# Kernel tuning notes

Measured on AMD Instinct MI355X. Metric: run time of the kernel, lower is better.

The kernel has to match this reference:

```python
import jax, jax.numpy as jnp
import numpy as np

DIM = 768
HEADS = 12
HEAD_DIM = DIM // HEADS
SCALE = HEAD_DIM ** -0.5


def setup_inputs() -> dict:
    key = jax.random.key(0)
    ks = jax.random.split(key, 5)
    x = jax.random.normal(ks[0], (2, 4096, DIM), dtype=jnp.float32)
    # torch nn.Linear params: weight [out, in], bias [out]
    qkv_w = jax.random.normal(ks[1], (3 * DIM, DIM), dtype=jnp.float32) * (DIM ** -0.5)
    qkv_b = jax.random.normal(ks[2], (3 * DIM,), dtype=jnp.float32) * 0.02
    proj_w = jax.random.normal(ks[3], (DIM, DIM), dtype=jnp.float32) * (DIM ** -0.5)
    proj_b = jax.random.normal(ks[4], (DIM,), dtype=jnp.float32) * 0.02
    return {"x": x, "qkv_w": qkv_w, "qkv_b": qkv_b, "proj_w": proj_w, "proj_b": proj_b}


def reference(x, qkv_w, qkv_b, proj_w, proj_b):
    b, n, c = x.shape
    qkv = x @ qkv_w.T + qkv_b                      # [b, n, 3c]
    qkv = qkv.reshape(b, n, 3, HEADS, HEAD_DIM)
    qkv = jnp.transpose(qkv, (2, 0, 3, 1, 4))      # [3, b, h, n, d]
    q, k, v = qkv[0], qkv[1], qkv[2]
    attn = jax.nn.softmax(jnp.einsum('bhqd,bhkd->bhqk', q, k) * SCALE, axis=-1)
    out = jnp.einsum('bhqk,bhkd->bhqd', attn, v)   # [b, h, n, d]
    out = jnp.transpose(out, (0, 2, 1, 3)).reshape(b, n, c)
    return out @ proj_w.T + proj_b
```

## Files before the change

### kernel.cpp

```cpp
#include <hip/hip_runtime.h>
#include <stdint.h>

#define SEQ   4096
#define NDIM  768
#define HD    64
#define NH    12
#define NBH   24
#define MTOT  8192

#define LSTR 40
#define PSTR 72

typedef short s8v __attribute__((ext_vector_type(8)));
typedef float f4v __attribute__((ext_vector_type(4)));
typedef float f16x __attribute__((ext_vector_type(16)));
typedef unsigned short u16;
typedef u16 u16x4 __attribute__((ext_vector_type(4)));
typedef uint32_t u32x4v __attribute__((ext_vector_type(4)));
typedef int i32x2 __attribute__((ext_vector_type(2)));

#define C1 0.18033688011112042f

__device__ __forceinline__ u16 f2bf(float f) {
  union { float f; uint32_t u; } cv; cv.f = f;
  const uint32_t u = cv.u;
  return (u16)((u + 0x7fffu + ((u >> 16) & 1u)) >> 16);
}
__device__ __forceinline__ float ex2(float x) { return __builtin_amdgcn_exp2f(x); }

__device__ __forceinline__ uint32_t cvtpk_bf16(float lo, float hi) {
  uint32_t r;
  asm("v_cvt_pk_bf16_f32 %0, %1, %2" : "=v"(r) : "v"(lo), "v"(hi));
  return r;
}
__device__ __forceinline__ void pl32swap(uint32_t& a, uint32_t& b) {
  i32x2 r = __builtin_amdgcn_permlane32_swap((int)a, (int)b, false, false);
  a = (uint32_t)r.x; b = (uint32_t)r.y;
}

__global__ __launch_bounds__(256) void cvt3_kernel(
    const float* __restrict__ a, u16* __restrict__ da, int na4,
    const float* __restrict__ b, u16* __restrict__ db, int nb4,
    const float* __restrict__ c, u16* __restrict__ dc, int nc4) {
  int i = blockIdx.x * 256 + threadIdx.x;
  const float* s; u16* d;
  if (i < na4)             { s = a; d = da; }
  else if (i < na4 + nb4)  { s = b; d = db; i -= na4; }
  else if (i < na4 + nb4 + nc4) { s = c; d = dc; i -= na4 + nb4; }
  else return;
  const float4 f = ((const float4*)s)[i];
  u16x4 r;
  r[0] = f2bf(f.x); r[1] = f2bf(f.y); r[2] = f2bf(f.z); r[3] = f2bf(f.w);
  ((u16x4*)d)[i] = r;
}

__global__ __launch_bounds__(256) void gemm_qkv(const u16* __restrict__ A,
    const u16* __restrict__ B, const float* __restrict__ bias,
    u16* __restrict__ qg, u16* __restrict__ kg, u16* __restrict__ vtg) {
  __shared__ __align__(16) u16 at[128 * LSTR];
  __shared__ __align__(16) u16 bt[128 * LSTR];
  const int tid  = threadIdx.x;
  const int lane = tid & 63;
  const int w    = tid >> 6;
  const int quad = lane >> 4;
  const int col  = lane & 15;
  const int m0 = blockIdx.y * 128;
  const int n0 = blockIdx.x * 128;
  const int srow = tid >> 2;
  const int sch  = (tid & 3) * 8;
  const int wm = (w >> 1) * 64;
  const int wn = (w & 1) * 64;

  const f4v fz = {0.f, 0.f, 0.f, 0.f};
  f4v acc[4][4];
#pragma unroll
  for (int i = 0; i < 4; i++)
#pragma unroll
    for (int j = 0; j < 4; j++) acc[i][j] = fz;

  const u16* ap0 = A + (size_t)(m0 + srow) * NDIM + sch;
  const u16* ap1 = A + (size_t)(m0 + 64 + srow) * NDIM + sch;
  const u16* bp0 = B + (size_t)(n0 + srow) * NDIM + sch;
  const u16* bp1 = B + (size_t)(n0 + 64 + srow) * NDIM + sch;

  for (int k0 = 0; k0 < NDIM; k0 += 32) {
    const s8v va0 = *(const s8v*)(ap0 + k0);
    const s8v va1 = *(const s8v*)(ap1 + k0);
    const s8v vb0 = *(const s8v*)(bp0 + k0);
    const s8v vb1 = *(const s8v*)(bp1 + k0);
    __syncthreads();
    *(s8v*)(at + srow * LSTR + sch) = va0;
    *(s8v*)(at + (64 + srow) * LSTR + sch) = va1;
    *(s8v*)(bt + srow * LSTR + sch) = vb0;
    *(s8v*)(bt + (64 + srow) * LSTR + sch) = vb1;
    __syncthreads();
    s8v af[4], bf[4];
#pragma unroll
    for (int i = 0; i < 4; i++)
      af[i] = *(const s8v*)(at + (wm + i * 16 + col) * LSTR + quad * 8);
#pragma unroll
    for (int j = 0; j < 4; j++)
      bf[j] = *(const s8v*)(bt + (wn + j * 16 + col) * LSTR + quad * 8);
#pragma unroll
    for (int i = 0; i < 4; i++)
#pragma unroll
      for (int j = 0; j < 4; j++)
        acc[i][j] = __builtin_amdgcn_mfma_f32_16x16x32_bf16(af[i], bf[j], acc[i][j], 0, 0, 0);
  }

  const int wmg = m0 + wm;
  const int wng = n0 + wn;
  const int s = n0 / NDIM;
#pragma unroll
  for (int j = 0; j < 4; j++) {
    const int c = wng + j * 16 + col;
    const float bv = bias[c];
    const int r = c - s * NDIM;
    const int h = r >> 6;
    const int d = r & 63;
#pragma unroll
    for (int i = 0; i < 4; i++) {
      const int mb = wmg + i * 16 + quad * 4;
      const int bb = mb >> 12;
      const int n  = mb & 4095;
      const size_t hb = (size_t)(bb * NH + h);
      const f4v v = acc[i][j];
      if (s == 2) {
        u16x4 pk;
#pragma unroll
        for (int rg = 0; rg < 4; rg++) pk[rg] = f2bf(v[rg] + bv);
        *(u16x4*)(vtg + (hb * HD + d) * SEQ + n) = pk;
      } else if (s == 0) {
#pragma unroll
        for (int rg = 0; rg < 4; rg++)
          qg[(hb * SEQ + (size_t)(n + rg)) * HD + d] = f2bf((v[rg] + bv) * C1);
      } else {
#pragma unroll
        for (int rg = 0; rg < 4; rg++)
          kg[(hb * SEQ + (size_t)(n + rg)) * HD + d] = f2bf(v[rg] + bv);
      }
    }
  }
}

__global__ __launch_bounds__(256, 3) void attn_kernel(const u16* __restrict__ qg,
    const u16* __restrict__ kg, const u16* __restrict__ vtg, u16* __restrict__ og) {
  __shared__ __align__(16) u16 kls[2][64 * PSTR];
  __shared__ __align__(16) u16 vls[2][64 * PSTR];
  __shared__ float lws[4][32];

  const int tid  = threadIdx.x;
  const int lane = tid & 63;
  const int w    = tid >> 6;
  const int hi   = lane >> 5;
  const int c    = lane & 31;
  const int blk = blockIdx.x;
  const int bh  = blk % NBH;
  const int q0  = (blk / NBH) * 128;
  const size_t gbase = (size_t)bh * (SEQ * HD);
  const int wq = w * 32;

  s8v qf[4];
#pragma unroll
  for (int s = 0; s < 4; s++)
    qf[s] = *(const s8v*)(qg + gbase + (size_t)(q0 + wq + c) * HD + s * 16 + hi * 8);

  f16x o0, o1;
#pragma unroll
  for (int e = 0; e < 16; e++) { o0[e] = 0.f; o1[e] = 0.f; }
  float l0 = 0.f, l1 = 0.f, l2 = 0.f, l3 = 0.f;

  const int srow8 = tid >> 3;
  const int sch8  = (tid & 7) * 8;
  const u16* kp = kg  + gbase + (size_t)srow8 * HD  + sch8;
  const u16* vp = vtg + gbase + (size_t)srow8 * SEQ;

  s8v kr0 = *(const s8v*)(kp);
  s8v kr1 = *(const s8v*)(kp + (size_t)32 * HD);
  s8v vr0 = *(const s8v*)(vp + sch8);
  s8v vr1 = *(const s8v*)(vp + (size_t)32 * SEQ + sch8);
  *(s8v*)(kls[0] + srow8 * PSTR + sch8) = kr0;
  *(s8v*)(kls[0] + (32 + srow8) * PSTR + sch8) = kr1;
  *(s8v*)(vls[0] + srow8 * PSTR + sch8) = vr0;
  *(s8v*)(vls[0] + (32 + srow8) * PSTR + sch8) = vr1;

  for (int kb = 0; kb < SEQ; kb += 64) {
    const int cur = (kb >> 6) & 1;
    const u16* kt_ = kls[cur];
    const u16* vt_ = vls[cur];
    __syncthreads();

    if (kb + 64 < SEQ) {
      kr0 = *(const s8v*)(kp + (size_t)(kb + 64) * HD);
      kr1 = *(const s8v*)(kp + (size_t)(kb + 96) * HD);
      vr0 = *(const s8v*)(vp + kb + 64 + sch8);
      vr1 = *(const s8v*)(vp + (size_t)32 * SEQ + kb + 64 + sch8);
    }

    f16x st0, st1;
#pragma unroll
    for (int e = 0; e < 16; e++) { st0[e] = 0.f; st1[e] = 0.f; }
#pragma unroll
    for (int s = 0; s < 4; s++) {
      const s8v k0 = *(const s8v*)(kt_ + c * PSTR + s * 16 + hi * 8);
      const s8v k1 = *(const s8v*)(kt_ + (32 + c) * PSTR + s * 16 + hi * 8);
      st0 = __builtin_amdgcn_mfma_f32_32x32x16_bf16(k0, qf[s], st0, 0, 0, 0);
      st1 = __builtin_amdgcn_mfma_f32_32x32x16_bf16(k1, qf[s], st1, 0, 0, 0);
    }

    s8v pa0, pa1, pa2, pa3;
    {
      float p[16];
#pragma unroll
      for (int e = 0; e < 16; e++) p[e] = ex2(st0[e]);
      l0 += p[0] + p[4] + p[8]  + p[12];
      l1 += p[1] + p[5] + p[9]  + p[13];
      l2 += p[2] + p[6] + p[10] + p[14];
      l3 += p[3] + p[7] + p[11] + p[15];
      uint32_t k0 = cvtpk_bf16(p[0],  p[1]);
      uint32_t k1 = cvtpk_bf16(p[2],  p[3]);
      uint32_t k2 = cvtpk_bf16(p[4],  p[5]);
      uint32_t k3 = cvtpk_bf16(p[6],  p[7]);
      uint32_t k4 = cvtpk_bf16(p[8],  p[9]);
      uint32_t k5 = cvtpk_bf16(p[10], p[11]);
      uint32_t k6 = cvtpk_bf16(p[12], p[13]);
      uint32_t k7 = cvtpk_bf16(p[14], p[15]);
      pl32swap(k0, k2); pl32swap(k1, k3);
      pl32swap(k4, k6); pl32swap(k5, k7);
      u32x4v wA = {k0, k1, k2, k3};
      u32x4v wB = {k4, k5, k6, k7};
      pa0 = __builtin_bit_cast(s8v, wA);
      pa1 = __builtin_bit_cast(s8v, wB);
    }
    {
      float p[16];
#pragma unroll
      for (int e = 0; e < 16; e++) p[e] = ex2(st1[e]);
      l0 += p[0] + p[4] + p[8]  + p[12];
      l1 += p[1] + p[5] + p[9]  + p[13];
      l2 += p[2] + p[6] + p[10] + p[14];
      l3 += p[3] + p[7] + p[11] + p[15];
      uint32_t k0 = cvtpk_bf16(p[0],  p[1]);
      uint32_t k1 = cvtpk_bf16(p[2],  p[3]);
      uint32_t k2 = cvtpk_bf16(p[4],  p[5]);
      uint32_t k3 = cvtpk_bf16(p[6],  p[7]);
      uint32_t k4 = cvtpk_bf16(p[8],  p[9]);
      uint32_t k5 = cvtpk_bf16(p[10], p[11]);
      uint32_t k6 = cvtpk_bf16(p[12], p[13]);
      uint32_t k7 = cvtpk_bf16(p[14], p[15]);
      pl32swap(k0, k2); pl32swap(k1, k3);
      pl32swap(k4, k6); pl32swap(k5, k7);
      u32x4v wA = {k0, k1, k2, k3};
      u32x4v wB = {k4, k5, k6, k7};
      pa2 = __builtin_bit_cast(s8v, wA);
      pa3 = __builtin_bit_cast(s8v, wB);
    }

#pragma unroll
    for (int ks = 0; ks < 4; ks++) {
      const s8v pv = ks == 0 ? pa0 : ks == 1 ? pa1 : ks == 2 ? pa2 : pa3;
      const s8v v0 = *(const s8v*)(vt_ + c * PSTR + ks * 16 + hi * 8);
      const s8v v1 = *(const s8v*)(vt_ + (32 + c) * PSTR + ks * 16 + hi * 8);
      o0 = __builtin_amdgcn_mfma_f32_32x32x16_bf16(pv, v0, o0, 0, 0, 0);
      o1 = __builtin_amdgcn_mfma_f32_32x32x16_bf16(pv, v1, o1, 0, 0, 0);
    }

    if (kb + 64 < SEQ) {
      u16* kn = (u16*)kls[cur ^ 1];
      u16* vn = (u16*)vls[cur ^ 1];
      *(s8v*)(kn + srow8 * PSTR + sch8) = kr0;
      *(s8v*)(kn + (32 + srow8) * PSTR + sch8) = kr1;
      *(s8v*)(vn + srow8 * PSTR + sch8) = vr0;
      *(s8v*)(vn + (32 + srow8) * PSTR + sch8) = vr1;
    }
  }

  float lt = l0 + l1 + l2 + l3;
  lt += __shfl_xor(lt, 32);
  const float inv = 1.0f / lt;
  if (hi == 0) lws[w][c] = inv;

  const int b = bh / NH;
  const int h = bh % NH;
  u16* obase = og + (size_t)(b * SEQ + q0 + wq) * NDIM + h * HD + c;
#pragma unroll
  for (int r = 0; r < 16; r++) {
    const int row = (r & 3) + 8 * (r >> 2) + 4 * hi;
    const float invr = lws[w][row];
    u16* rp = obase + (size_t)row * NDIM;
    rp[0]  = f2bf(o0[r] * invr);
    rp[32] = f2bf(o1[r] * invr);
  }
}

__global__ __launch_bounds__(256) void gemm_proj(const u16* __restrict__ A,
    const u16* __restrict__ B, const float* __restrict__ bias, float* __restrict__ out) {
  __shared__ __align__(16) u16 at[128 * LSTR];
  __shared__ __align__(16) u16 bt[128 * LSTR];
  const int tid  = threadIdx.x;
  const int lane = tid & 63;
  const int w    = tid >> 6;
  const int quad = lane >> 4;
  const int col  = lane & 15;
  const int m0 = blockIdx.y * 128;
  const int n0 = blockIdx.x * 128;
  const int srow = tid >> 2;
  const int sch  = (tid & 3) * 8;
  const int wm = (w >> 1) * 64;
  const int wn = (w & 1) * 64;

  const f4v fz = {0.f, 0.f, 0.f, 0.f};
  f4v acc[4][4];
#pragma unroll
  for (int i = 0; i < 4; i++)
#pragma unroll
    for (int j = 0; j < 4; j++) acc[i][j] = fz;

  const u16* ap0 = A + (size_t)(m0 + srow) * NDIM + sch;
  const u16* ap1 = A + (size_t)(m0 + 64 + srow) * NDIM + sch;
  const u16* bp0 = B + (size_t)(n0 + srow) * NDIM + sch;
  const u16* bp1 = B + (size_t)(n0 + 64 + srow) * NDIM + sch;

  for (int k0 = 0; k0 < NDIM; k0 += 32) {
    const s8v va0 = *(const s8v*)(ap0 + k0);
    const s8v va1 = *(const s8v*)(ap1 + k0);
    const s8v vb0 = *(const s8v*)(bp0 + k0);
    const s8v vb1 = *(const s8v*)(bp1 + k0);
    __syncthreads();
    *(s8v*)(at + srow * LSTR + sch) = va0;
    *(s8v*)(at + (64 + srow) * LSTR + sch) = va1;
    *(s8v*)(bt + srow * LSTR + sch) = vb0;
    *(s8v*)(bt + (64 + srow) * LSTR + sch) = vb1;
    __syncthreads();
    s8v af[4], bf[4];
#pragma unroll
    for (int i = 0; i < 4; i++)
      af[i] = *(const s8v*)(at + (wm + i * 16 + col) * LSTR + quad * 8);
#pragma unroll
    for (int j = 0; j < 4; j++)
      bf[j] = *(const s8v*)(bt + (wn + j * 16 + col) * LSTR + quad * 8);
#pragma unroll
    for (int i = 0; i < 4; i++)
#pragma unroll
      for (int j = 0; j < 4; j++)
        acc[i][j] = __builtin_amdgcn_mfma_f32_16x16x32_bf16(af[i], bf[j], acc[i][j], 0, 0, 0);
  }

  const int wmg = m0 + wm;
  const int wng = n0 + wn;
#pragma unroll
  for (int j = 0; j < 4; j++) {
    const int c = wng + j * 16 + col;
    const float bv = bias[c];
#pragma unroll
    for (int i = 0; i < 4; i++) {
#pragma unroll
      for (int rg = 0; rg < 4; rg++)
        out[(size_t)(wmg + i * 16 + quad * 4 + rg) * NDIM + c] = acc[i][j][rg] + bv;
    }
  }
}

extern "C" void kernel_launch(void* const* d_in, const int* in_sizes, int n_in,
                              void* d_out, int out_size, void* d_ws, size_t ws_size,
                              hipStream_t stream) {
  const float* x      = (const float*)d_in[0];
  const float* qkv_w  = (const float*)d_in[1];
  const float* qkv_b  = (const float*)d_in[2];
  const float* proj_w = (const float*)d_in[3];
  const float* proj_b = (const float*)d_in[4];
  float* out = (float*)d_out;

  u16* ws   = (u16*)d_ws;
  u16* x_bf = ws;
  u16* wq   = x_bf + (size_t)MTOT * NDIM;
  u16* wp   = wq + (size_t)3 * NDIM * NDIM;
  u16* q_bf = wp + (size_t)NDIM * NDIM;
  u16* k_bf = q_bf + (size_t)NBH * SEQ * HD;
  u16* vt   = k_bf + (size_t)NBH * SEQ * HD;
  u16* a_bf = vt + (size_t)NBH * SEQ * HD;

  const int nx = MTOT * NDIM / 4, nw1 = 3 * NDIM * NDIM / 4, nw2 = NDIM * NDIM / 4;
  const int ntot = nx + nw1 + nw2;
  cvt3_kernel<<<(ntot + 255) / 256, 256, 0, stream>>>(x, x_bf, nx, qkv_w, wq, nw1,
                                                      proj_w, wp, nw2);

  gemm_qkv<<<dim3(18, 64), 256, 0, stream>>>(x_bf, wq, qkv_b, q_bf, k_bf, vt);
  attn_kernel<<<768, 256, 0, stream>>>(q_bf, k_bf, vt, a_bf);
  gemm_proj<<<dim3(6, 64), 256, 0, stream>>>(a_bf, wp, proj_b, out);
}
```

Measured before the change: 285.2 us.

## Load K fragments directly into registers and interleave softmax with PV MFMAs

K tiles are no longer staged through shared memory. Each lane loads its MFMA K fragments straight from global memory into registers, one tile ahead, which removes the K LDS stores and reads and halves shared-memory use. The PV matmul is split into two halves that are interleaved with the exp/convert work of each score block, and the MFMA sections are wrapped in s_setprio to favour matrix issue. The cost is more global-load traffic per wave, since lanes read overlapping K rows without reuse across waves, plus extra register pressure from the eight prefetched K fragments.

```diff
diff --git a/kernel.cpp b/kernel.cpp
--- a/kernel.cpp
+++ b/kernel.cpp
@@ -145,7 +145,6 @@
 
 __global__ __launch_bounds__(256, 3) void attn_kernel(const u16* __restrict__ qg,
     const u16* __restrict__ kg, const u16* __restrict__ vtg, u16* __restrict__ og) {
-  __shared__ __align__(16) u16 kls[2][64 * PSTR];
   __shared__ __align__(16) u16 vls[2][64 * PSTR];
   __shared__ float lws[4][32];
 
@@ -165,47 +164,58 @@
   for (int s = 0; s < 4; s++)
     qf[s] = *(const s8v*)(qg + gbase + (size_t)(q0 + wq + c) * HD + s * 16 + hi * 8);
 
-  f16x o0, o1;
-#pragma unroll
-  for (int e = 0; e < 16; e++) { o0[e] = 0.f; o1[e] = 0.f; }
+  const u16* kq0 = kg + gbase + (size_t)c * HD + hi * 8;
+  const u16* kq1 = kq0 + (size_t)32 * HD;
+  s8v kf0[4], kf1[4];
+#pragma unroll
+  for (int s = 0; s < 4; s++) {
+    kf0[s] = *(const s8v*)(kq0 + s * 16);
+    kf1[s] = *(const s8v*)(kq1 + s * 16);
+  }
+
+  f16x zacc;
+#pragma unroll
+  for (int e = 0; e < 16; e++) zacc[e] = 0.f;
+  f16x o0 = zacc, o1 = zacc;
   float l0 = 0.f, l1 = 0.f, l2 = 0.f, l3 = 0.f;
 
   const int srow8 = tid >> 3;
   const int sch8  = (tid & 7) * 8;
-  const u16* kp = kg  + gbase + (size_t)srow8 * HD  + sch8;
   const u16* vp = vtg + gbase + (size_t)srow8 * SEQ;
 
-  s8v kr0 = *(const s8v*)(kp);
-  s8v kr1 = *(const s8v*)(kp + (size_t)32 * HD);
   s8v vr0 = *(const s8v*)(vp + sch8);
   s8v vr1 = *(const s8v*)(vp + (size_t)32 * SEQ + sch8);
-  *(s8v*)(kls[0] + srow8 * PSTR + sch8) = kr0;
-  *(s8v*)(kls[0] + (32 + srow8) * PSTR + sch8) = kr1;
   *(s8v*)(vls[0] + srow8 * PSTR + sch8) = vr0;
   *(s8v*)(vls[0] + (32 + srow8) * PSTR + sch8) = vr1;
 
   for (int kb = 0; kb < SEQ; kb += 64) {
     const int cur = (kb >> 6) & 1;
-    const u16* kt_ = kls[cur];
     const u16* vt_ = vls[cur];
     __syncthreads();
 
     if (kb + 64 < SEQ) {
-      kr0 = *(const s8v*)(kp + (size_t)(kb + 64) * HD);
-      kr1 = *(const s8v*)(kp + (size_t)(kb + 96) * HD);
       vr0 = *(const s8v*)(vp + kb + 64 + sch8);
       vr1 = *(const s8v*)(vp + (size_t)32 * SEQ + kb + 64 + sch8);
     }
 
-    f16x st0, st1;
-#pragma unroll
-    for (int e = 0; e < 16; e++) { st0[e] = 0.f; st1[e] = 0.f; }
-#pragma unroll
-    for (int s = 0; s < 4; s++) {
-      const s8v k0 = *(const s8v*)(kt_ + c * PSTR + s * 16 + hi * 8);
-      const s8v k1 = *(const s8v*)(kt_ + (32 + c) * PSTR + s * 16 + hi * 8);
-      st0 = __builtin_amdgcn_mfma_f32_32x32x16_bf16(k0, qf[s], st0, 0, 0, 0);
-      st1 = __builtin_amdgcn_mfma_f32_32x32x16_bf16(k1, qf[s], st1, 0, 0, 0);
+    __builtin_amdgcn_s_setprio(1);
+    f16x st0 = __builtin_amdgcn_mfma_f32_32x32x16_bf16(kf0[0], qf[0], zacc, 0, 0, 0);
+    f16x st1 = __builtin_amdgcn_mfma_f32_32x32x16_bf16(kf1[0], qf[0], zacc, 0, 0, 0);
+#pragma unroll
+    for (int s = 1; s < 4; s++) {
+      st0 = __builtin_amdgcn_mfma_f32_32x32x16_bf16(kf0[s], qf[s], st0, 0, 0, 0);
+      st1 = __builtin_amdgcn_mfma_f32_32x32x16_bf16(kf1[s], qf[s], st1, 0, 0, 0);
+    }
+    __builtin_amdgcn_s_setprio(0);
+
+    if (kb + 64 < SEQ) {
+      const u16* nk0 = kq0 + (size_t)(kb + 64) * HD;
+      const u16* nk1 = kq1 + (size_t)(kb + 64) * HD;
+#pragma unroll
+      for (int s = 0; s < 4; s++) {
+        kf0[s] = *(const s8v*)(nk0 + s * 16);
+        kf1[s] = *(const s8v*)(nk1 + s * 16);
+      }
     }
 
     s8v pa0, pa1, pa2, pa3;
@@ -232,6 +242,20 @@
       pa0 = __builtin_bit_cast(s8v, wA);
       pa1 = __builtin_bit_cast(s8v, wB);
     }
+
+    __builtin_amdgcn_s_setprio(1);
+    {
+      const s8v v00 = *(const s8v*)(vt_ + c * PSTR + hi * 8);
+      const s8v v01 = *(const s8v*)(vt_ + (32 + c) * PSTR + hi * 8);
+      const s8v v10 = *(const s8v*)(vt_ + c * PSTR + 16 + hi * 8);
+      const s8v v11 = *(const s8v*)(vt_ + (32 + c) * PSTR + 16 + hi * 8);
+      o0 = __builtin_amdgcn_mfma_f32_32x32x16_bf16(pa0, v00, o0, 0, 0, 0);
+      o1 = __builtin_amdgcn_mfma_f32_32x32x16_bf16(pa0, v01, o1, 0, 0, 0);
+      o0 = __builtin_amdgcn_mfma_f32_32x32x16_bf16(pa1, v10, o0, 0, 0, 0);
+      o1 = __builtin_amdgcn_mfma_f32_32x32x16_bf16(pa1, v11, o1, 0, 0, 0);
+    }
+    __builtin_amdgcn_s_setprio(0);
+
     {
       float p[16];
 #pragma unroll
@@ -256,23 +280,24 @@
       pa3 = __builtin_bit_cast(s8v, wB);
     }
 
-#pragma unroll
-    for (int ks = 0; ks < 4; ks++) {
-      const s8v pv = ks == 0 ? pa0 : ks == 1 ? pa1 : ks == 2 ? pa2 : pa3;
-      const s8v v0 = *(const s8v*)(vt_ + c * PSTR + ks * 16 + hi * 8);
-      const s8v v1 = *(const s8v*)(vt_ + (32 + c) * PSTR + ks * 16 + hi * 8);
-      o0 = __builtin_amdgcn_mfma_f32_32x32x16_bf16(pv, v0, o0, 0, 0, 0);
-      o1 = __builtin_amdgcn_mfma_f32_32x32x16_bf16(pv, v1, o1, 0, 0, 0);
-    }
-
     if (kb + 64 < SEQ) {
-      u16* kn = (u16*)kls[cur ^ 1];
       u16* vn = (u16*)vls[cur ^ 1];
-      *(s8v*)(kn + srow8 * PSTR + sch8) = kr0;
-      *(s8v*)(kn + (32 + srow8) * PSTR + sch8) = kr1;
       *(s8v*)(vn + srow8 * PSTR + sch8) = vr0;
       *(s8v*)(vn + (32 + srow8) * PSTR + sch8) = vr1;
     }
+
+    __builtin_amdgcn_s_setprio(1);
+    {
+      const s8v v20 = *(const s8v*)(vt_ + c * PSTR + 32 + hi * 8);
+      const s8v v21 = *(const s8v*)(vt_ + (32 + c) * PSTR + 32 + hi * 8);
+      const s8v v30 = *(const s8v*)(vt_ + c * PSTR + 48 + hi * 8);
+      const s8v v31 = *(const s8v*)(vt_ + (32 + c) * PSTR + 48 + hi * 8);
+      o0 = __builtin_amdgcn_mfma_f32_32x32x16_bf16(pa2, v20, o0, 0, 0, 0);
+      o1 = __builtin_amdgcn_mfma_f32_32x32x16_bf16(pa2, v21, o1, 0, 0, 0);
+      o0 = __builtin_amdgcn_mfma_f32_32x32x16_bf16(pa3, v30, o0, 0, 0, 0);
+      o1 = __builtin_amdgcn_mfma_f32_32x32x16_bf16(pa3, v31, o1, 0, 0, 0);
+    }
+    __builtin_amdgcn_s_setprio(0);
   }
 
   float lt = l0 + l1 + l2 + l3;
```

Result: slower. 358.3 us (+25.6%).

## Use direct global-to-LDS loads with XOR swizzle in GEMMs and interleave PV MFMAs

Applied to the files above, without the earlier changes.

Both projection GEMMs now stage tiles with global_load_lds (16-byte direct-to-LDS loads), which bypasses VGPRs. The tiles use an unpadded XOR-swizzled layout to avoid bank conflicts. In the attention kernel, the P·V MFMAs are split into two halves interleaved with the second softmax exp block and the next-tile LDS stores, and the MFMA phases are wrapped in s_setprio. The goal is lower staging overhead and better overlap of MFMA with VALU work. The GEMM loop still waits synchronously on each load with no prefetch, and the direct LDS load relies on the swizzle mapping and per-wave base being right.

```diff
diff --git a/kernel.cpp b/kernel.cpp
--- a/kernel.cpp
+++ b/kernel.cpp
@@ -8,7 +8,6 @@
 #define NBH   24
 #define MTOT  8192
 
-#define LSTR 40
 #define PSTR 72
 
 typedef short s8v __attribute__((ext_vector_type(8)));
@@ -36,6 +35,11 @@
 __device__ __forceinline__ void pl32swap(uint32_t& a, uint32_t& b) {
   i32x2 r = __builtin_amdgcn_permlane32_swap((int)a, (int)b, false, false);
   a = (uint32_t)r.x; b = (uint32_t)r.y;
+}
+__device__ __forceinline__ void gload_lds16(const void* g, void* l) {
+  __builtin_amdgcn_global_load_lds(
+      (const __attribute__((address_space(1))) uint32_t*)g,
+      (__attribute__((address_space(3))) uint32_t*)l, 16, 0, 0);
 }
 
 __global__ __launch_bounds__(256) void cvt3_kernel(
@@ -57,8 +61,8 @@
 __global__ __launch_bounds__(256) void gemm_qkv(const u16* __restrict__ A,
     const u16* __restrict__ B, const float* __restrict__ bias,
     u16* __restrict__ qg, u16* __restrict__ kg, u16* __restrict__ vtg) {
-  __shared__ __align__(16) u16 at[128 * LSTR];
-  __shared__ __align__(16) u16 bt[128 * LSTR];
+  __shared__ __align__(16) u16 at[128 * 32];
+  __shared__ __align__(16) u16 bt[128 * 32];
   const int tid  = threadIdx.x;
   const int lane = tid & 63;
   const int w    = tid >> 6;
@@ -67,9 +71,10 @@
   const int m0 = blockIdx.y * 128;
   const int n0 = blockIdx.x * 128;
   const int srow = tid >> 2;
-  const int sch  = (tid & 3) * 8;
+  const int schk = ((tid & 3) ^ (srow & 3)) * 8;
   const int wm = (w >> 1) * 64;
   const int wn = (w & 1) * 64;
+  const int xq = (quad ^ (col & 3)) * 8;
 
   const f4v fz = {0.f, 0.f, 0.f, 0.f};
   f4v acc[4][4];
@@ -78,29 +83,27 @@
 #pragma unroll
     for (int j = 0; j < 4; j++) acc[i][j] = fz;
 
-  const u16* ap0 = A + (size_t)(m0 + srow) * NDIM + sch;
-  const u16* ap1 = A + (size_t)(m0 + 64 + srow) * NDIM + sch;
-  const u16* bp0 = B + (size_t)(n0 + srow) * NDIM + sch;
-  const u16* bp1 = B + (size_t)(n0 + 64 + srow) * NDIM + sch;
+  const u16* ga0 = A + (size_t)(m0 + srow) * NDIM + schk;
+  const u16* ga1 = A + (size_t)(m0 + 64 + srow) * NDIM + schk;
+  const u16* gb0 = B + (size_t)(n0 + srow) * NDIM + schk;
+  const u16* gb1 = B + (size_t)(n0 + 64 + srow) * NDIM + schk;
+  u16* const la = at + (size_t)w * 512;
+  u16* const lb = bt + (size_t)w * 512;
 
   for (int k0 = 0; k0 < NDIM; k0 += 32) {
-    const s8v va0 = *(const s8v*)(ap0 + k0);
-    const s8v va1 = *(const s8v*)(ap1 + k0);
-    const s8v vb0 = *(const s8v*)(bp0 + k0);
-    const s8v vb1 = *(const s8v*)(bp1 + k0);
     __syncthreads();
-    *(s8v*)(at + srow * LSTR + sch) = va0;
-    *(s8v*)(at + (64 + srow) * LSTR + sch) = va1;
-    *(s8v*)(bt + srow * LSTR + sch) = vb0;
-    *(s8v*)(bt + (64 + srow) * LSTR + sch) = vb1;
+    gload_lds16(ga0 + k0, la);
+    gload_lds16(ga1 + k0, la + 2048);
+    gload_lds16(gb0 + k0, lb);
+    gload_lds16(gb1 + k0, lb + 2048);
     __syncthreads();
     s8v af[4], bf[4];
 #pragma unroll
     for (int i = 0; i < 4; i++)
-      af[i] = *(const s8v*)(at + (wm + i * 16 + col) * LSTR + quad * 8);
+      af[i] = *(const s8v*)(at + (wm + i * 16 + col) * 32 + xq);
 #pragma unroll
     for (int j = 0; j < 4; j++)
-      bf[j] = *(const s8v*)(bt + (wn + j * 16 + col) * LSTR + quad * 8);
+      bf[j] = *(const s8v*)(bt + (wn + j * 16 + col) * 32 + xq);
 #pragma unroll
     for (int i = 0; i < 4; i++)
 #pragma unroll
@@ -200,6 +203,7 @@
     f16x st0, st1;
 #pragma unroll
     for (int e = 0; e < 16; e++) { st0[e] = 0.f; st1[e] = 0.f; }
+    __builtin_amdgcn_s_setprio(1);
 #pragma unroll
     for (int s = 0; s < 4; s++) {
       const s8v k0 = *(const s8v*)(kt_ + c * PSTR + s * 16 + hi * 8);
@@ -207,6 +211,7 @@
       st0 = __builtin_amdgcn_mfma_f32_32x32x16_bf16(k0, qf[s], st0, 0, 0, 0);
       st1 = __builtin_amdgcn_mfma_f32_32x32x16_bf16(k1, qf[s], st1, 0, 0, 0);
     }
+    __builtin_amdgcn_s_setprio(0);
 
     s8v pa0, pa1, pa2, pa3;
     {
@@ -232,6 +237,20 @@
       pa0 = __builtin_bit_cast(s8v, wA);
       pa1 = __builtin_bit_cast(s8v, wB);
     }
+
+    __builtin_amdgcn_s_setprio(1);
+    {
+      const s8v v00 = *(const s8v*)(vt_ + c * PSTR + hi * 8);
+      const s8v v01 = *(const s8v*)(vt_ + (32 + c) * PSTR + hi * 8);
+      const s8v v10 = *(const s8v*)(vt_ + c * PSTR + 16 + hi * 8);
+      const s8v v11 = *(const s8v*)(vt_ + (32 + c) * PSTR + 16 + hi * 8);
+      o0 = __builtin_amdgcn_mfma_f32_32x32x16_bf16(pa0, v00, o0, 0, 0, 0);
+      o1 = __builtin_amdgcn_mfma_f32_32x32x16_bf16(pa0, v01, o1, 0, 0, 0);
+      o0 = __builtin_amdgcn_mfma_f32_32x32x16_bf16(pa1, v10, o0, 0, 0, 0);
+      o1 = __builtin_amdgcn_mfma_f32_32x32x16_bf16(pa1, v11, o1, 0, 0, 0);
+    }
+    __builtin_amdgcn_s_setprio(0);
+
     {
       float p[16];
 #pragma unroll
@@ -256,15 +275,6 @@
       pa3 = __builtin_bit_cast(s8v, wB);
     }
 
-#pragma unroll
-    for (int ks = 0; ks < 4; ks++) {
-      const s8v pv = ks == 0 ? pa0 : ks == 1 ? pa1 : ks == 2 ? pa2 : pa3;
-      const s8v v0 = *(const s8v*)(vt_ + c * PSTR + ks * 16 + hi * 8);
-      const s8v v1 = *(const s8v*)(vt_ + (32 + c) * PSTR + ks * 16 + hi * 8);
-      o0 = __builtin_amdgcn_mfma_f32_32x32x16_bf16(pv, v0, o0, 0, 0, 0);
-      o1 = __builtin_amdgcn_mfma_f32_32x32x16_bf16(pv, v1, o1, 0, 0, 0);
-    }
-
     if (kb + 64 < SEQ) {
       u16* kn = (u16*)kls[cur ^ 1];
       u16* vn = (u16*)vls[cur ^ 1];
@@ -273,6 +283,19 @@
       *(s8v*)(vn + srow8 * PSTR + sch8) = vr0;
       *(s8v*)(vn + (32 + srow8) * PSTR + sch8) = vr1;
     }
+
+    __builtin_amdgcn_s_setprio(1);
+    {
+      const s8v v20 = *(const s8v*)(vt_ + c * PSTR + 32 + hi * 8);
+      const s8v v21 = *(const s8v*)(vt_ + (32 + c) * PSTR + 32 + hi * 8);
+      const s8v v30 = *(const s8v*)(vt_ + c * PSTR + 48 + hi * 8);
+      const s8v v31 = *(const s8v*)(vt_ + (32 + c) * PSTR + 48 + hi * 8);
+      o0 = __builtin_amdgcn_mfma_f32_32x32x16_bf16(pa2, v20, o0, 0, 0, 0);
+      o1 = __builtin_amdgcn_mfma_f32_32x32x16_bf16(pa2, v21, o1, 0, 0, 0);
+      o0 = __builtin_amdgcn_mfma_f32_32x32x16_bf16(pa3, v30, o0, 0, 0, 0);
+      o1 = __builtin_amdgcn_mfma_f32_32x32x16_bf16(pa3, v31, o1, 0, 0, 0);
+    }
+    __builtin_amdgcn_s_setprio(0);
   }
 
   float lt = l0 + l1 + l2 + l3;
@@ -295,8 +318,8 @@
 
 __global__ __launch_bounds__(256) void gemm_proj(const u16* __restrict__ A,
     const u16* __restrict__ B, const float* __restrict__ bias, float* __restrict__ out) {
-  __shared__ __align__(16) u16 at[128 * LSTR];
-  __shared__ __align__(16) u16 bt[128 * LSTR];
+  __shared__ __align__(16) u16 at[128 * 32];
+  __shared__ __align__(16) u16 bt[128 * 32];
   const int tid  = threadIdx.x;
   const int lane = tid & 63;
   const int w    = tid >> 6;
@@ -305,9 +328,10 @@
   const int m0 = blockIdx.y * 128;
   const int n0 = blockIdx.x * 128;
   const int srow = tid >> 2;
-  const int sch  = (tid & 3) * 8;
+  const int schk = ((tid & 3) ^ (srow & 3)) * 8;
   const int wm = (w >> 1) * 64;
   const int wn = (w & 1) * 64;
+  const int xq = (quad ^ (col & 3)) * 8;
 
   const f4v fz = {0.f, 0.f, 0.f, 0.f};
   f4v acc[4][4];
@@ -316,29 +340,27 @@
 #pragma unroll
     for (int j = 0; j < 4; j++) acc[i][j] = fz;
 
-  const u16* ap0 = A + (size_t)(m0 + srow) * NDIM + sch;
-  const u16* ap1 = A + (size_t)(m0 + 64 + srow) * NDIM + sch;
-  const u16* bp0 = B + (size_t)(n0 + srow) * NDIM + sch;
-  const u16* bp1 = B + (size_t)(n0 + 64 + srow) * NDIM + sch;
+  const u16* ga0 = A + (size_t)(m0 + srow) * NDIM + schk;
+  const u16* ga1 = A + (size_t)(m0 + 64 + srow) * NDIM + schk;
+  const u16* gb0 = B + (size_t)(n0 + srow) * NDIM + schk;
+  const u16* gb1 = B + (size_t)(n0 + 64 + srow) * NDIM + schk;
+  u16* const la = at + (size_t)w * 512;
+  u16* const lb = bt + (size_t)w * 512;
 
   for (int k0 = 0; k0 < NDIM; k0 += 32) {
-    const s8v va0 = *(const s8v*)(ap0 + k0);
-    const s8v va1 = *(const s8v*)(ap1 + k0);
-    const s8v vb0 = *(const s8v*)(bp0 + k0);
-    const s8v vb1 = *(const s8v*)(bp1 + k0);
     __syncthreads();
-    *(s8v*)(at + srow * LSTR + sch) = va0;
-    *(s8v*)(at + (64 + srow) * LSTR + sch) = va1;
-    *(s8v*)(bt + srow * LSTR + sch) = vb0;
-    *(s8v*)(bt + (64 + srow) * LSTR + sch) = vb1;
+    gload_lds16(ga0 + k0, la);
+    gload_lds16(ga1 + k0, la + 2048);
+    gload_lds16(gb0 + k0, lb);
+    gload_lds16(gb1 + k0, lb + 2048);
     __syncthreads();
     s8v af[4], bf[4];
 #pragma unroll
     for (int i = 0; i < 4; i++)
-      af[i] = *(const s8v*)(at + (wm + i * 16 + col) * LSTR + quad * 8);
+      af[i] = *(const s8v*)(at + (wm + i * 16 + col) * 32 + xq);
 #pragma unroll
     for (int j = 0; j < 4; j++)
-      bf[j] = *(const s8v*)(bt + (wn + j * 16 + col) * LSTR + quad * 8);
+      bf[j] = *(const s8v*)(bt + (wn + j * 16 + col) * 32 + xq);
 #pragma unroll
     for (int i = 0; i < 4; i++)
 #pragma unroll
```

New measurement: 278.8 us. 1.02x faster.
